# Kernel tuning notes

Hardware: AMD Instinct MI355X
Metric: run time of the kernel (lower is better)

## Reference

```python
import jax, jax.numpy as jnp
import numpy as np

N = 50000          # nodes
E = 800000         # edges (before self loops)
F_IN = 16
HID = 64
HEADS = 4
C = 64             # per-head out channels (concat=False)
G = 64             # graphs in batch
NEG_SLOPE = 0.2


def setup_inputs() -> dict:
    key = jax.random.key(0)
    ks = jax.random.split(key, 20)
    inp = {
        "x": jax.random.normal(ks[0], (N, F_IN), jnp.float32),
        "edge_index": jax.random.randint(ks[1], (2, E), 0, N, jnp.int64),
        "batch": jnp.sort(jax.random.randint(ks[2], (N,), 0, G, jnp.int64)),
        "W_in": jax.random.normal(ks[3], (HID, F_IN), jnp.float32) * 0.1,
        "b_in": jnp.zeros((HID,), jnp.float32),
        "W_out": jax.random.normal(ks[4], (1, HID), jnp.float32) * 0.1,
        "b_out": jnp.zeros((1,), jnp.float32),
    }
    for l in range(3):
        inp[f"W{l}"] = jax.random.normal(ks[5 + 4 * l], (HEADS * C, HID), jnp.float32) * 0.1
        inp[f"asrc{l}"] = jax.random.normal(ks[6 + 4 * l], (HEADS, C), jnp.float32) * 0.1
        inp[f"adst{l}"] = jax.random.normal(ks[7 + 4 * l], (HEADS, C), jnp.float32) * 0.1
        inp[f"bg{l}"] = jnp.zeros((HID,), jnp.float32)
    return inp


def _gat_layer(x, W, a_src, a_dst, bias, src, dst, n):
    # x: [N, HID] -> h: [N, HEADS, C]
    h = (x @ W.T).reshape(n, HEADS, C)
    alpha_s = jnp.einsum("nhc,hc->nh", h, a_src)   # [N, H]
    alpha_d = jnp.einsum("nhc,hc->nh", h, a_dst)
    e = jax.nn.leaky_relu(alpha_s[src] + alpha_d[dst], NEG_SLOPE)  # [E', H]
    # segment softmax over incoming edges of each dst node
    m = jax.ops.segment_max(e, dst, num_segments=n)
    e = jnp.exp(e - m[dst])
    s = jax.ops.segment_sum(e, dst, num_segments=n)
    alpha = e / (s[dst] + 1e-16)                                   # [E', H]
    msg = alpha[:, :, None] * h[src]                               # [E', H, C]
    out = jax.ops.segment_sum(msg, dst, num_segments=n)            # [N, H, C]
    return out.mean(axis=1) + bias                                 # concat=False: head mean


def reference(x, W_in, b_in, W0, asrc0, adst0, bg0, W1, asrc1, adst1, bg1,
              W2, asrc2, adst2, bg2, W_out, b_out, edge_index, batch):
    n = x.shape[0]
    # add self loops (PyG GATConv default)
    loops = jnp.arange(n, dtype=edge_index.dtype)
    src = jnp.concatenate([edge_index[0], loops])
    dst = jnp.concatenate([edge_index[1], loops])

    h = x @ W_in.T + b_in
    for W, a_s, a_d, bg in ((W0, asrc0, adst0, bg0),
                            (W1, asrc1, adst1, bg1),
                            (W2, asrc2, adst2, bg2)):
        h = jax.nn.relu(_gat_layer(h, W, a_s, a_d, bg, src, dst, n))
        # dropout p=0.2 is inactive in eval mode

    # global mean pool over graphs
    sums = jax.ops.segment_sum(h, batch, num_segments=G)
    cnt = jax.ops.segment_sum(jnp.ones((n,), h.dtype), batch, num_segments=G)
    graph_emb = sums / jnp.maximum(cnt, 1.0)[:, None]              # [G, HID]

    return jax.nn.sigmoid(graph_emb @ W_out.T + b_out)             # [G, 1]
```

## Files before the change

### kernel.cpp

```cpp
#include <hip/hip_runtime.h>
#include <hip/hip_bf16.h>
#include <hip/hip_fp16.h>

#define HID 64
#define HEADS 4
#define GCNT 64
#define F_IN 16
#define NEG 0.2f
#define NBUCK 256
#define BSLOT 6144
#define SCHUNK 2048

typedef _Float16 f16x8 __attribute__((ext_vector_type(8)));
typedef float f32x4 __attribute__((ext_vector_type(4)));

__device__ __forceinline__ unsigned pack_h2(float a, float b) {
  __half2 h = __floats2half2_rn(a, b);
  union { __half2 h; unsigned u; } c;
  c.h = h;
  return c.u;
}
__device__ __forceinline__ __half2 uas_h2(unsigned u) {
  union { unsigned u; __half2 h; } c;
  c.u = u;
  return c.h;
}
__device__ __forceinline__ unsigned h2_as_u(__half2 h) {
  union { __half2 h; unsigned u; } c;
  c.h = h;
  return c.u;
}
__device__ __forceinline__ __half2 xor16_add(__half2 v) {
  unsigned u = (unsigned)__shfl_xor((int)h2_as_u(v), 16, 64);
  return __hadd2(v, uas_h2(u));
}

__global__ __launch_bounds__(256) void k_pre(
    const float* __restrict__ W0, const float* __restrict__ asrc,
    const float* __restrict__ adst, const float* __restrict__ Win,
    const float* __restrict__ bin, int* __restrict__ bcur,
    float* __restrict__ vb, float* __restrict__ c8) {
  int t = threadIdx.x;
  if (blockIdx.x == 0) {
    bcur[t] = 0;
    return;
  }
  __shared__ float vaL[512];
#pragma unroll
  for (int it = 0; it < 2; ++it) {
    int idx = t + it * 256;
    int q = idx >> 6, j = idx & 63;
    const float* a = (q < 4) ? asrc : adst;
    int h = q & 3;
    float s = 0.f;
    for (int c = 0; c < 64; ++c) s += a[h * 64 + c] * W0[(h * 64 + c) * 64 + j];
    vaL[idx] = s;
  }
  __syncthreads();
  if (t < 128) {
    int q = t >> 4, k = t & 15;
    float s = 0.f;
    for (int j = 0; j < 64; ++j) s += vaL[q * 64 + j] * Win[j * F_IN + k];
    vb[t] = s;
  } else if (t < 136) {
    int q = t - 128;
    float s = 0.f;
    for (int j = 0; j < 64; ++j) s += vaL[q * 64 + j] * bin[j];
    c8[q] = s;
  }
}

__global__ __launch_bounds__(256) void k_bucket(
    const int* __restrict__ ei, int* __restrict__ bcur,
    unsigned* __restrict__ tmp, int E, int N) {
  __shared__ int hist[NBUCK];
  __shared__ int base[NBUCK];
  int t = threadIdx.x;
  int start = blockIdx.x * SCHUNK;
  int end = min(start + SCHUNK, E + N);
  hist[t] = 0;
  __syncthreads();
  unsigned val[8];
  int rank[8];
  bool ok[8];
#pragma unroll
  for (int k = 0; k < 8; ++k) {
    int i = start + t + k * 256;
    ok[k] = i < end;
    if (ok[k]) {
      int s, d;
      if (i < E) {
        s = ei[i];
        d = ei[E + i];
      } else {
        s = d = i - E;
      }
      val[k] = ((unsigned)d << 16) | (unsigned)s;
      rank[k] = atomicAdd(&hist[d >> 8], 1);
    }
  }
  __syncthreads();
  int h = hist[t];
  base[t] = h ? atomicAdd(&bcur[t], h) : 0;
  __syncthreads();
#pragma unroll
  for (int k = 0; k < 8; ++k) {
    if (ok[k]) {
      int bk = (int)(val[k] >> 24);
      int idx = base[bk] + rank[k];
      if (idx < BSLOT) tmp[(size_t)bk * BSLOT + idx] = val[k];
    }
  }
}

__global__ __launch_bounds__(256) void k_bsort(
    const unsigned* __restrict__ tmp, const int* __restrict__ bcur,
    int* __restrict__ rowptr, int* __restrict__ col, int N) {
  __shared__ int s[NBUCK];
  __shared__ int hist[NBUCK];
  __shared__ int pref[NBUCK];
  int b = blockIdx.x, t = threadIdx.x;
  int c = min(bcur[t], BSLOT);
  s[t] = c;
  __syncthreads();
  for (int o = 1; o < 256; o <<= 1) {
    int x = (t >= o) ? s[t - o] : 0;
    __syncthreads();
    s[t] += x;
    __syncthreads();
  }
  int base = (b == 0) ? 0 : s[b - 1];
  int total = s[255];
  int cntb = min(bcur[b], BSLOT);
  hist[t] = 0;
  __syncthreads();
  for (int j = t; j < cntb; j += 256)
    atomicAdd(&hist[(tmp[(size_t)b * BSLOT + j] >> 16) & 255], 1);
  __syncthreads();
  int v = hist[t];
  pref[t] = v;
  __syncthreads();
  for (int o = 1; o < 256; o <<= 1) {
    int x = (t >= o) ? pref[t - o] : 0;
    __syncthreads();
    pref[t] += x;
    __syncthreads();
  }
  pref[t] -= v;
  __syncthreads();
  int node = b * 256 + t;
  if (node < N) rowptr[node] = base + pref[t];
  if (b == 255 && t == 255) rowptr[N] = total;
  hist[t] = 0;
  __syncthreads();
  for (int j = t; j < cntb; j += 256) {
    unsigned e = tmp[(size_t)b * BSLOT + j];
    int d8 = (int)((e >> 16) & 255);
    int r = atomicAdd(&hist[d8], 1);
    col[base + pref[d8] + r] = (int)(e & 0xffffu);
  }
}

__global__ void k_init(const float* __restrict__ x, const float* __restrict__ Win,
                       const float* __restrict__ bin,
                       const float* __restrict__ W0, const float* __restrict__ W1,
                       const float* __restrict__ W2,
                       __half* __restrict__ Wh3, __half* __restrict__ Wcat3,
                       float* __restrict__ sums, const float* __restrict__ vb,
                       const float* __restrict__ c8,
                       float* __restrict__ as_, float* __restrict__ ad_,
                       __half* __restrict__ hh, int N) {
  int b = blockIdx.x, t = threadIdx.x;
  if (b < 384) {
    int i = b * 256 + t;
    if (i < 49152) {
      const float* W = (i < 16384) ? W0 : (i < 32768) ? W1 : W2;
      Wh3[i] = __float2half(W[i & 16383]);
    } else {
      int j = i - 49152;
      int l = j >> 14;
      int r = j & 16383;
      int c = r >> 8;
      int k256 = r & 255;
      int h = k256 & 3, kk = k256 >> 2;
      const float* W = (l == 0) ? W0 : (l == 1) ? W1 : W2;
      Wcat3[j] = __float2half(0.25f * W[(h * 64 + c) * 64 + kk]);
    }
    return;
  }
  if (b < 401) {
    int i = (b - 384) * 256 + t;
    if (i < GCNT * HID + GCNT) sums[i] = 0.f;
    return;
  }
  int i = (b - 401) * 256 + t;
  if (i >= N * HID) return;
  int n = i >> 6, j = i & 63;
  const float* xr = x + (size_t)n * F_IN;
  const float* wr = Win + j * F_IN;
  float xv[F_IN];
  float acc = bin[j];
#pragma unroll
  for (int k = 0; k < F_IN; ++k) {
    xv[k] = xr[k];
    acc = fmaf(xv[k], wr[k], acc);
  }
  hh[i] = __float2half(acc);
  if (j < 8) {
    const float* vbq = vb + j * 16;
    float s = c8[j];
#pragma unroll
    for (int k = 0; k < F_IN; ++k) s = fmaf(xv[k], vbq[k], s);
    if (j < 4) as_[(size_t)n * 4 + j] = s;
    else ad_[(size_t)n * 4 + (j - 4)] = s;
  }
}

__device__ __forceinline__ void gat_one_node(
    int node, int lane, const __half* __restrict__ h, const float* __restrict__ as_,
    const float* __restrict__ ad_, const int* __restrict__ rowptr,
    const int* __restrict__ col, __half* __restrict__ Mrow) {
  int r0 = rowptr[node];
  int deg = rowptr[node + 1] - r0;
  float4 adv = *(const float4*)(ad_ + (size_t)node * 4);

  if (deg <= 64) {
    int off = 0;
    float x0 = 0.f, x1 = 0.f, x2 = 0.f, x3 = 0.f;
    if (lane < deg) {
      int s = col[r0 + lane];
      off = s << 6;
      float4 av = *(const float4*)(as_ + (size_t)s * 4);
      float e0 = av.x + adv.x; e0 = (e0 > 0.f) ? e0 : NEG * e0;
      float e1 = av.y + adv.y; e1 = (e1 > 0.f) ? e1 : NEG * e1;
      float e2 = av.z + adv.z; e2 = (e2 > 0.f) ? e2 : NEG * e2;
      float e3 = av.w + adv.w; e3 = (e3 > 0.f) ? e3 : NEG * e3;
      x0 = __expf(fminf(e0, 60.f));
      x1 = __expf(fminf(e1, 60.f));
      x2 = __expf(fminf(e2, 60.f));
      x3 = __expf(fminf(e3, 60.f));
    }
    float s0 = x0, s1 = x1, s2 = x2, s3 = x3;
#pragma unroll
    for (int o = 32; o; o >>= 1) {
      s0 += __shfl_xor(s0, o, 64);
      s1 += __shfl_xor(s1, o, 64);
      s2 += __shfl_xor(s2, o, 64);
      s3 += __shfl_xor(s3, o, 64);
    }
    unsigned w01 = pack_h2(x0 / (s0 + 1e-16f), x1 / (s1 + 1e-16f));
    unsigned w23 = pack_h2(x2 / (s2 + 1e-16f), x3 / (s3 + 1e-16f));
    __half2 acc01 = __floats2half2_rn(0.f, 0.f);
    __half2 acc23 = acc01;
#pragma unroll 4
    for (int j = 0; j < deg; ++j) {
      int oj = __builtin_amdgcn_readlane(off, j) + lane;
      unsigned W01 = __builtin_amdgcn_readlane(w01, j);
      unsigned W23 = __builtin_amdgcn_readlane(w23, j);
      __half2 hv = __half2half2(h[oj]);
      acc01 = __hfma2(hv, uas_h2(W01), acc01);
      acc23 = __hfma2(hv, uas_h2(W23), acc23);
    }
    *(__half2*)&Mrow[lane * 4] = acc01;
    *(__half2*)&Mrow[lane * 4 + 2] = acc23;
    return;
  }
  float m0 = -1e30f, m1 = -1e30f, m2 = -1e30f, m3 = -1e30f;
  for (int j = lane; j < deg; j += 64) {
    int s = col[r0 + j];
    float4 av = *(const float4*)(as_ + (size_t)s * 4);
    float e0 = av.x + adv.x; e0 = (e0 > 0.f) ? e0 : NEG * e0; m0 = fmaxf(m0, e0);
    float e1 = av.y + adv.y; e1 = (e1 > 0.f) ? e1 : NEG * e1; m1 = fmaxf(m1, e1);
    float e2 = av.z + adv.z; e2 = (e2 > 0.f) ? e2 : NEG * e2; m2 = fmaxf(m2, e2);
    float e3 = av.w + adv.w; e3 = (e3 > 0.f) ? e3 : NEG * e3; m3 = fmaxf(m3, e3);
  }
#pragma unroll
  for (int o = 32; o; o >>= 1) {
    m0 = fmaxf(m0, __shfl_xor(m0, o, 64));
    m1 = fmaxf(m1, __shfl_xor(m1, o, 64));
    m2 = fmaxf(m2, __shfl_xor(m2, o, 64));
    m3 = fmaxf(m3, __shfl_xor(m3, o, 64));
  }
  float s0 = 0.f, s1 = 0.f, s2 = 0.f, s3 = 0.f;
  for (int j = lane; j < deg; j += 64) {
    int s = col[r0 + j];
    float4 av = *(const float4*)(as_ + (size_t)s * 4);
    float e0 = av.x + adv.x; e0 = (e0 > 0.f) ? e0 : NEG * e0; s0 += __expf(e0 - m0);
    float e1 = av.y + adv.y; e1 = (e1 > 0.f) ? e1 : NEG * e1; s1 += __expf(e1 - m1);
    float e2 = av.z + adv.z; e2 = (e2 > 0.f) ? e2 : NEG * e2; s2 += __expf(e2 - m2);
    float e3 = av.w + adv.w; e3 = (e3 > 0.f) ? e3 : NEG * e3; s3 += __expf(e3 - m3);
  }
#pragma unroll
  for (int o = 32; o; o >>= 1) {
    s0 += __shfl_xor(s0, o, 64);
    s1 += __shfl_xor(s1, o, 64);
    s2 += __shfl_xor(s2, o, 64);
    s3 += __shfl_xor(s3, o, 64);
  }
  float i0 = 1.f / (s0 + 1e-16f), i1 = 1.f / (s1 + 1e-16f);
  float i2 = 1.f / (s2 + 1e-16f), i3 = 1.f / (s3 + 1e-16f);
  float a0 = 0.f, a1 = 0.f, a2 = 0.f, a3 = 0.f;
  for (int j = 0; j < deg; ++j) {
    int s = col[r0 + j];
    float4 av = *(const float4*)(as_ + (size_t)s * 4);
    float e0 = av.x + adv.x; e0 = (e0 > 0.f) ? e0 : NEG * e0;
    float e1 = av.y + adv.y; e1 = (e1 > 0.f) ? e1 : NEG * e1;
    float e2 = av.z + adv.z; e2 = (e2 > 0.f) ? e2 : NEG * e2;
    float e3 = av.w + adv.w; e3 = (e3 > 0.f) ? e3 : NEG * e3;
    float hv = __half2float(h[(s << 6) + lane]);
    a0 = fmaf(__expf(e0 - m0) * i0, hv, a0);
    a1 = fmaf(__expf(e1 - m1) * i1, hv, a1);
    a2 = fmaf(__expf(e2 - m2) * i2, hv, a2);
    a3 = fmaf(__expf(e3 - m3) * i3, hv, a3);
  }
  *(__half2*)&Mrow[lane * 4] = __floats2half2_rn(a0, a1);
  *(__half2*)&Mrow[lane * 4 + 2] = __floats2half2_rn(a2, a3);
}

__device__ __forceinline__ void gat_pair(
    int pr, int lane, int half, int l5, int N,
    const __half* __restrict__ h, const float* __restrict__ as_,
    const float* __restrict__ ad_, const int* __restrict__ rowptr,
    const int* __restrict__ col, __half* __restrict__ Mt) {
  int n0 = pr * 2;
  int n1 = min(n0 + 1, N - 1);
  int mynode = half ? n1 : n0;
  int r0 = rowptr[mynode];
  int dg = rowptr[mynode + 1] - r0;
  int dgA = __builtin_amdgcn_readlane(dg, 0);
  int dgB = __builtin_amdgcn_readlane(dg, 32);

  if (dgA <= 32 && dgB <= 32) {
    float4 adv = *(const float4*)(ad_ + (size_t)mynode * 4);
    int off = 0;
    float x0 = 0.f, x1 = 0.f, x2 = 0.f, x3 = 0.f;
    if (l5 < dg) {
      int s = col[r0 + l5];
      off = s << 6;
      float4 av = *(const float4*)(as_ + (size_t)s * 4);
      float e0 = av.x + adv.x; e0 = (e0 > 0.f) ? e0 : NEG * e0;
      float e1 = av.y + adv.y; e1 = (e1 > 0.f) ? e1 : NEG * e1;
      float e2 = av.z + adv.z; e2 = (e2 > 0.f) ? e2 : NEG * e2;
      float e3 = av.w + adv.w; e3 = (e3 > 0.f) ? e3 : NEG * e3;
      x0 = __expf(fminf(e0, 60.f));
      x1 = __expf(fminf(e1, 60.f));
      x2 = __expf(fminf(e2, 60.f));
      x3 = __expf(fminf(e3, 60.f));
    }
    float s0 = x0, s1 = x1, s2 = x2, s3 = x3;
#pragma unroll
    for (int o = 16; o; o >>= 1) {
      s0 += __shfl_xor(s0, o, 64);
      s1 += __shfl_xor(s1, o, 64);
      s2 += __shfl_xor(s2, o, 64);
      s3 += __shfl_xor(s3, o, 64);
    }
    unsigned w01 = pack_h2(x0 / (s0 + 1e-16f), x1 / (s1 + 1e-16f));
    unsigned w23 = pack_h2(x2 / (s2 + 1e-16f), x3 / (s3 + 1e-16f));

    int g = l5 >> 4, li = l5 & 15;
    const uint2* h4p = (const uint2*)h;
    __half2 z = __floats2half2_rn(0.f, 0.f);
    __half2 a0_01 = z, a0_23 = z, a1_01 = z, a1_23 = z;
    __half2 a2_01 = z, a2_23 = z, a3_01 = z, a3_23 = z;
    int mdeg = max(dgA, dgB);
    int baddr = half << 7;
#pragma unroll 2
    for (int j = 0; j < mdeg; j += 2) {
      int addr = baddr + (j + g) * 4;
      int oj = __builtin_amdgcn_ds_bpermute(addr, off);
      unsigned W01 = (unsigned)__builtin_amdgcn_ds_bpermute(addr, (int)w01);
      unsigned W23 = (unsigned)__builtin_amdgcn_ds_bpermute(addr, (int)w23);
      uint2 hv = h4p[(oj >> 2) + li];
      __half2 ha = uas_h2(hv.x), hb = uas_h2(hv.y);
      __half2 wA = uas_h2(W01), wB = uas_h2(W23);
      __half2 c0 = __low2half2(ha), c1 = __high2half2(ha);
      __half2 c2 = __low2half2(hb), c3 = __high2half2(hb);
      a0_01 = __hfma2(c0, wA, a0_01); a0_23 = __hfma2(c0, wB, a0_23);
      a1_01 = __hfma2(c1, wA, a1_01); a1_23 = __hfma2(c1, wB, a1_23);
      a2_01 = __hfma2(c2, wA, a2_01); a2_23 = __hfma2(c2, wB, a2_23);
      a3_01 = __hfma2(c3, wA, a3_01); a3_23 = __hfma2(c3, wB, a3_23);
    }
    a0_01 = xor16_add(a0_01); a0_23 = xor16_add(a0_23);
    a1_01 = xor16_add(a1_01); a1_23 = xor16_add(a1_23);
    a2_01 = xor16_add(a2_01); a2_23 = xor16_add(a2_23);
    a3_01 = xor16_add(a3_01); a3_23 = xor16_add(a3_23);
    if (g == 0) {
      __half* row = &Mt[(mynode & 15) * 264 + li * 16];
      uint4 st1, st2;
      st1.x = h2_as_u(a0_01); st1.y = h2_as_u(a0_23);
      st1.z = h2_as_u(a1_01); st1.w = h2_as_u(a1_23);
      st2.x = h2_as_u(a2_01); st2.y = h2_as_u(a2_23);
      st2.z = h2_as_u(a3_01); st2.w = h2_as_u(a3_23);
      *(uint4*)&row[0] = st1;
      *(uint4*)&row[8] = st2;
    }
  } else {
    gat_one_node(n0, lane, h, as_, ad_, rowptr, col, &Mt[(n0 & 15) * 264]);
    if (n1 != n0) gat_one_node(n1, lane, h, as_, ad_, rowptr, col, &Mt[(n1 & 15) * 264]);
  }
}

template <bool FIN>
__global__ __launch_bounds__(256) void k_gatf(
    const __half* __restrict__ h, const float* __restrict__ as_,
    const float* __restrict__ ad_, const int* __restrict__ rowptr,
    const int* __restrict__ col, const __half* __restrict__ Wcat,
    const float* __restrict__ bg, const __half* __restrict__ Wn,
    const float* __restrict__ asrc, const float* __restrict__ adst,
    __half* __restrict__ hout, float* __restrict__ nas, float* __restrict__ nad,
    const int* __restrict__ batchv, float* __restrict__ gsums,
    int N) {
  __shared__ __half Mt[16 * 264];
  __shared__ __half O[16 * 72];
  int tid = threadIdx.x;
  int lane = tid & 63, wv = tid >> 6;
  int tile = blockIdx.x;
  int half = lane >> 5, l5 = lane & 31;
  int npairs = (N + 1) >> 1;

  int pr0 = tile * 8 + wv * 2;
  int pr1 = pr0 + 1;
  bool has0 = pr0 < npairs, has1 = pr1 < npairs;
  if (has0 && has1) {
    int my0 = min(pr0 * 2 + half, N - 1);
    int my1 = min(pr1 * 2 + half, N - 1);
    int r0a = rowptr[my0];
    int dga = rowptr[my0 + 1] - r0a;
    int r0b = rowptr[my1];
    int dgb = rowptr[my1 + 1] - r0b;
    int dA0 = __builtin_amdgcn_readlane(dga, 0);
    int dB0 = __builtin_amdgcn_readlane(dga, 32);
    int dA1 = __builtin_amdgcn_readlane(dgb, 0);
    int dB1 = __builtin_amdgcn_readlane(dgb, 32);

    if (dA0 <= 32 && dB0 <= 32 && dA1 <= 32 && dB1 <= 32) {
      float4 adva = *(const float4*)(ad_ + (size_t)my0 * 4);
      float4 advb = *(const float4*)(ad_ + (size_t)my1 * 4);
      int offa = 0, offb = 0;
      float xa0 = 0.f, xa1 = 0.f, xa2 = 0.f, xa3 = 0.f;
      float xb0 = 0.f, xb1 = 0.f, xb2 = 0.f, xb3 = 0.f;
      if (l5 < dga) {
        int s = col[r0a + l5];
        offa = s << 6;
        float4 av = *(const float4*)(as_ + (size_t)s * 4);
        float e0 = av.x + adva.x; e0 = (e0 > 0.f) ? e0 : NEG * e0;
        float e1 = av.y + adva.y; e1 = (e1 > 0.f) ? e1 : NEG * e1;
        float e2 = av.z + adva.z; e2 = (e2 > 0.f) ? e2 : NEG * e2;
        float e3 = av.w + adva.w; e3 = (e3 > 0.f) ? e3 : NEG * e3;
        xa0 = __expf(fminf(e0, 60.f));
        xa1 = __expf(fminf(e1, 60.f));
        xa2 = __expf(fminf(e2, 60.f));
        xa3 = __expf(fminf(e3, 60.f));
      }
      if (l5 < dgb) {
        int s = col[r0b + l5];
        offb = s << 6;
        float4 av = *(const float4*)(as_ + (size_t)s * 4);
        float e0 = av.x + advb.x; e0 = (e0 > 0.f) ? e0 : NEG * e0;
        float e1 = av.y + advb.y; e1 = (e1 > 0.f) ? e1 : NEG * e1;
        float e2 = av.z + advb.z; e2 = (e2 > 0.f) ? e2 : NEG * e2;
        float e3 = av.w + advb.w; e3 = (e3 > 0.f) ? e3 : NEG * e3;
        xb0 = __expf(fminf(e0, 60.f));
        xb1 = __expf(fminf(e1, 60.f));
        xb2 = __expf(fminf(e2, 60.f));
        xb3 = __expf(fminf(e3, 60.f));
      }
      float sa0 = xa0, sa1 = xa1, sa2 = xa2, sa3 = xa3;
      float sb0 = xb0, sb1 = xb1, sb2 = xb2, sb3 = xb3;
#pragma unroll
      for (int o = 16; o; o >>= 1) {
        sa0 += __shfl_xor(sa0, o, 64);
        sa1 += __shfl_xor(sa1, o, 64);
        sa2 += __shfl_xor(sa2, o, 64);
        sa3 += __shfl_xor(sa3, o, 64);
        sb0 += __shfl_xor(sb0, o, 64);
        sb1 += __shfl_xor(sb1, o, 64);
        sb2 += __shfl_xor(sb2, o, 64);
        sb3 += __shfl_xor(sb3, o, 64);
      }
      unsigned w01a = pack_h2(xa0 / (sa0 + 1e-16f), xa1 / (sa1 + 1e-16f));
      unsigned w23a = pack_h2(xa2 / (sa2 + 1e-16f), xa3 / (sa3 + 1e-16f));
      unsigned w01b = pack_h2(xb0 / (sb0 + 1e-16f), xb1 / (sb1 + 1e-16f));
      unsigned w23b = pack_h2(xb2 / (sb2 + 1e-16f), xb3 / (sb3 + 1e-16f));

      uint4* EB = (uint4*)&Mt[wv * 1056];
      EB[half * 32 + l5] = make_uint4((unsigned)offa, w01a, w23a, 0u);
      EB[64 + half * 32 + l5] = make_uint4((unsigned)offb, w01b, w23b, 0u);

      int g = l5 >> 4, li = l5 & 15;
      const uint2* h4p = (const uint2*)h;
      __half2 z = __floats2half2_rn(0.f, 0.f);
      __half2 pa0 = z, pa1 = z, pa2 = z, pa3 = z, pa4 = z, pa5 = z, pa6 = z, pa7 = z;
      __half2 pb0 = z, pb1 = z, pb2 = z, pb3 = z, pb4 = z, pb5 = z, pb6 = z, pb7 = z;
      int mm = max(max(dA0, dB0), max(dA1, dB1));
      int ebase = half * 32;
#pragma unroll 2
      for (int j = 0; j < mm; j += 2) {
        uint4 ra = EB[ebase + j + g];
        uint4 rb = EB[64 + ebase + j + g];
        uint2 hva = h4p[((int)ra.x >> 2) + li];
        uint2 hvb = h4p[((int)rb.x >> 2) + li];
        {
          __half2 ha = uas_h2(hva.x), hb = uas_h2(hva.y);
          __half2 wA = uas_h2(ra.y), wB = uas_h2(ra.z);
          __half2 c0 = __low2half2(ha), c1 = __high2half2(ha);
          __half2 c2 = __low2half2(hb), c3 = __high2half2(hb);
          pa0 = __hfma2(c0, wA, pa0); pa1 = __hfma2(c0, wB, pa1);
          pa2 = __hfma2(c1, wA, pa2); pa3 = __hfma2(c1, wB, pa3);
          pa4 = __hfma2(c2, wA, pa4); pa5 = __hfma2(c2, wB, pa5);
          pa6 = __hfma2(c3, wA, pa6); pa7 = __hfma2(c3, wB, pa7);
        }
        {
          __half2 ha = uas_h2(hvb.x), hb = uas_h2(hvb.y);
          __half2 wA = uas_h2(rb.y), wB = uas_h2(rb.z);
          __half2 c0 = __low2half2(ha), c1 = __high2half2(ha);
          __half2 c2 = __low2half2(hb), c3 = __high2half2(hb);
          pb0 = __hfma2(c0, wA, pb0); pb1 = __hfma2(c0, wB, pb1);
          pb2 = __hfma2(c1, wA, pb2); pb3 = __hfma2(c1, wB, pb3);
          pb4 = __hfma2(c2, wA, pb4); pb5 = __hfma2(c2, wB, pb5);
          pb6 = __hfma2(c3, wA, pb6); pb7 = __hfma2(c3, wB, pb7);
        }
      }
      pa0 = xor16_add(pa0); pa1 = xor16_add(pa1); pa2 = xor16_add(pa2); pa3 = xor16_add(pa3);
      pa4 = xor16_add(pa4); pa5 = xor16_add(pa5); pa6 = xor16_add(pa6); pa7 = xor16_add(pa7);
      pb0 = xor16_add(pb0); pb1 = xor16_add(pb1); pb2 = xor16_add(pb2); pb3 = xor16_add(pb3);
      pb4 = xor16_add(pb4); pb5 = xor16_add(pb5); pb6 = xor16_add(pb6); pb7 = xor16_add(pb7);
      if (g == 0) {
        __half* rowA = &Mt[(my0 & 15) * 264 + li * 16];
        __half* rowB = &Mt[(my1 & 15) * 264 + li * 16];
        uint4 s1, s2;
        s1.x = h2_as_u(pa0); s1.y = h2_as_u(pa1); s1.z = h2_as_u(pa2); s1.w = h2_as_u(pa3);
        s2.x = h2_as_u(pa4); s2.y = h2_as_u(pa5); s2.z = h2_as_u(pa6); s2.w = h2_as_u(pa7);
        *(uint4*)&rowA[0] = s1;
        *(uint4*)&rowA[8] = s2;
        s1.x = h2_as_u(pb0); s1.y = h2_as_u(pb1); s1.z = h2_as_u(pb2); s1.w = h2_as_u(pb3);
        s2.x = h2_as_u(pb4); s2.y = h2_as_u(pb5); s2.z = h2_as_u(pb6); s2.w = h2_as_u(pb7);
        *(uint4*)&rowB[0] = s1;
        *(uint4*)&rowB[8] = s2;
      }
    } else {
      gat_pair(pr0, lane, half, l5, N, h, as_, ad_, rowptr, col, Mt);
      gat_pair(pr1, lane, half, l5, N, h, as_, ad_, rowptr, col, Mt);
    }
  } else if (has0) {
    gat_pair(pr0, lane, half, l5, N, h, as_, ad_, rowptr, col, Mt);
  }
  __syncthreads();

  int quad = lane >> 4, n16 = lane & 15;
  const f16x8* WC = (const f16x8*)Wcat;
  int ch1 = wv * 16 + n16;
  float bias1 = bg[ch1];
  f32x4 c1 = {0.f, 0.f, 0.f, 0.f};
#pragma unroll
  for (int i = 0; i < 8; ++i) {
    f16x8 a = *(const f16x8*)&Mt[n16 * 264 + (i * 4 + quad) * 8];
    c1 = __builtin_amdgcn_mfma_f32_16x16x32_f16(a, WC[ch1 * 32 + i * 4 + quad], c1, 0, 0, 0);
  }
#pragma unroll
  for (int r = 0; r < 4; ++r) {
    float v = fmaxf(c1[r] + bias1, 0.f);
    O[(quad * 4 + r) * 72 + ch1] = __float2half(v);
  }
  __syncthreads();

  if (FIN) {
    if (tid < 64) {
      float* cnt_ = gsums + GCNT * HID;
      int c = tid;
      int nmax = min(16, N - tile * 16);
      int curg = -1;
      float acc = 0.f;
      int cacc = 0;
      for (int i = 0; i < nmax; ++i) {
        int gph = batchv[tile * 16 + i];
        float v = __half2float(O[i * 72 + c]);
        if (gph != curg) {
          if (curg >= 0) {
            atomicAdd(&gsums[curg * HID + c], acc);
            if (c == 0) atomicAdd(&cnt_[curg], (float)cacc);
          }
          curg = gph;
          acc = 0.f;
          cacc = 0;
        }
        acc += v;
        ++cacc;
      }
      if (curg >= 0) {
        atomicAdd(&gsums[curg * HID + c], acc);
        if (c == 0) atomicAdd(&cnt_[curg], (float)cacc);
      }
    }
    return;
  }

  {
    int nd = tid >> 4, c0 = (tid & 15) * 4;
    int node = tile * 16 + nd;
    if (node < N) {
      uint2 v = *(const uint2*)&O[nd * 72 + c0];
      *(uint2*)&hout[(size_t)node * 64 + c0] = v;
    }
  }
  {
    const f16x8* WN = (const f16x8*)Wn;
    f16x8 a0 = *(const f16x8*)&O[n16 * 72 + quad * 8];
    f16x8 a1 = *(const f16x8*)&O[n16 * 72 + 32 + quad * 8];
    f32x4 accs[4];
#pragma unroll
    for (int nt = 0; nt < 4; ++nt) {
      int ch = wv * 64 + nt * 16 + n16;
      f32x4 zz = {0.f, 0.f, 0.f, 0.f};
      zz = __builtin_amdgcn_mfma_f32_16x16x32_f16(a0, WN[ch * 8 + quad], zz, 0, 0, 0);
      zz = __builtin_amdgcn_mfma_f32_16x16x32_f16(a1, WN[ch * 8 + 4 + quad], zz, 0, 0, 0);
      accs[nt] = zz;
    }
#pragma unroll
    for (int r = 0; r < 4; ++r) {
      float vs = 0.f, vd = 0.f;
#pragma unroll
      for (int nt = 0; nt < 4; ++nt) {
        int ch = wv * 64 + nt * 16 + n16;
        vs = fmaf(accs[nt][r], asrc[ch], vs);
        vd = fmaf(accs[nt][r], adst[ch], vd);
      }
#pragma unroll
      for (int o = 8; o; o >>= 1) {
        vs += __shfl_xor(vs, o, 64);
        vd += __shfl_xor(vd, o, 64);
      }
      int node = tile * 16 + quad * 4 + r;
      if (n16 == 0 && node < N) {
        nas[(size_t)node * 4 + wv] = vs;
        nad[(size_t)node * 4 + wv] = vd;
      }
    }
  }
}

__global__ void k_out(const float* __restrict__ sums, const float* __restrict__ cnt,
                      const float* __restrict__ Wout, const float* __restrict__ bout,
                      float* __restrict__ out) {
  int g = blockIdx.x, lane = threadIdx.x;
  float cg = fmaxf(cnt[g], 1.f);
  float v = (sums[g * HID + lane] / cg) * Wout[lane];
#pragma unroll
  for (int o = 32; o; o >>= 1) v += __shfl_xor(v, o, 64);
  if (lane == 0) out[g] = 1.f / (1.f + __expf(-v));
}

extern "C" void kernel_launch(void* const* d_in, const int* in_sizes, int n_in,
                              void* d_out, int out_size, void* d_ws, size_t ws_size,
                              hipStream_t stream) {
  const float* x    = (const float*)d_in[0];
  const int*   ei   = (const int*)d_in[1];
  const int*   batch= (const int*)d_in[2];
  const float* Win  = (const float*)d_in[3];
  const float* bin  = (const float*)d_in[4];
  const float* Wout = (const float*)d_in[5];
  const float* bout = (const float*)d_in[6];
  const float* Wl[3]    = {(const float*)d_in[7],  (const float*)d_in[11], (const float*)d_in[15]};
  const float* asrcl[3] = {(const float*)d_in[8],  (const float*)d_in[12], (const float*)d_in[16]};
  const float* adstl[3] = {(const float*)d_in[9],  (const float*)d_in[13], (const float*)d_in[17]};
  const float* bgl[3]   = {(const float*)d_in[10], (const float*)d_in[14], (const float*)d_in[18]};

  int N = in_sizes[2];
  int E = in_sizes[1] / 2;
  int EE = E + N;

  char* p = (char*)d_ws;
  auto alloc = [&](size_t bytes) {
    char* r = p;
    p += (bytes + 255) & ~(size_t)255;
    return r;
  };
  int*      rowptr = (int*)alloc((size_t)(N + 1) * 4);
  int*      col    = (int*)alloc((size_t)EE * 4);
  unsigned* tmp    = (unsigned*)alloc((size_t)NBUCK * BSLOT * 4);
  int*      bcur   = (int*)alloc(NBUCK * 4);
  float*    vb     = (float*)alloc(128 * 4);
  float*    c8     = (float*)alloc(8 * 4);
  __half*   hhA    = (__half*)alloc((size_t)N * HID * 2);
  __half*   hhB    = (__half*)alloc((size_t)N * HID * 2);
  float*    asA    = (float*)alloc((size_t)N * HEADS * 4);
  float*    adA    = (float*)alloc((size_t)N * HEADS * 4);
  float*    asB    = (float*)alloc((size_t)N * HEADS * 4);
  float*    adB    = (float*)alloc((size_t)N * HEADS * 4);
  __half*   Wh3    = (__half*)alloc(3 * 16384 * 2);
  __half*   Wcat3  = (__half*)alloc(3 * 16384 * 2);
  float*    sums   = (float*)alloc((size_t)(GCNT * HID + GCNT) * 4);
  float*    cnt    = sums + GCNT * HID;

  int tiles = (N + 15) / 16;

  k_pre<<<2, 256, 0, stream>>>(Wl[0], asrcl[0], adstl[0], Win, bin, bcur, vb, c8);
  k_bucket<<<(EE + SCHUNK - 1) / SCHUNK, 256, 0, stream>>>(ei, bcur, tmp, E, N);
  k_bsort<<<NBUCK, 256, 0, stream>>>(tmp, bcur, rowptr, col, N);

  k_init<<<401 + (N * HID + 255) / 256, 256, 0, stream>>>(
      x, Win, bin, Wl[0], Wl[1], Wl[2], Wh3, Wcat3, sums, vb, c8, asA, adA, hhA, N);

  k_gatf<false><<<tiles, 256, 0, stream>>>(hhA, asA, adA, rowptr, col,
                                           Wcat3, bgl[0], Wh3 + 16384, asrcl[1], adstl[1],
                                           hhB, asB, adB, nullptr, nullptr, N);
  k_gatf<false><<<tiles, 256, 0, stream>>>(hhB, asB, adB, rowptr, col,
                                           Wcat3 + 16384, bgl[1], Wh3 + 32768, asrcl[2], adstl[2],
                                           hhA, asA, adA, nullptr, nullptr, N);
  k_gatf<true><<<tiles, 256, 0, stream>>>(hhA, asA, adA, rowptr, col,
                                          Wcat3 + 32768, bgl[2], nullptr, nullptr, nullptr,
                                          nullptr, nullptr, nullptr, batch, sums, N);

  k_out<<<GCNT, 64, 0, stream>>>(sums, cnt, Wout, bout, (float*)d_out);
}
```

Before: 314.6 us.

## Merge bucketing into init kernel and add 16-byte gather variant for GAT aggregation

Fuses the edge bucketing kernel with the feature/weight init kernel into one launch, using block-index ranges so the two independent jobs run concurrently and one launch disappears. Adds a templated aggregation variant where each lane gathers 16 bytes of a neighbour row (8 lanes per row, 4 edges per step), reducing with xor-8 and xor-16 shuffles. The wider variant is used for layers 0 and 2 and the old 8-byte path for layer 1. It uses more accumulator registers, which may lower occupancy, and clamps the edge index for padded slots.

```diff
diff --git a/kernel.cpp b/kernel.cpp
--- a/kernel.cpp
+++ b/kernel.cpp
@@ -34,6 +34,20 @@
   unsigned u = (unsigned)__shfl_xor((int)h2_as_u(v), 16, 64);
   return __hadd2(v, uas_h2(u));
 }
+__device__ __forceinline__ __half2 xor8_16_add(__half2 v) {
+  unsigned u = (unsigned)__shfl_xor((int)h2_as_u(v), 8, 64);
+  v = __hadd2(v, uas_h2(u));
+  u = (unsigned)__shfl_xor((int)h2_as_u(v), 16, 64);
+  return __hadd2(v, uas_h2(u));
+}
+
+#define EXP_U(U, W01, W23, A0, A1, A2, A3)                      \
+  do {                                                          \
+    __half2 _h = uas_h2(U);                                     \
+    __half2 _cl = __low2half2(_h), _ch = __high2half2(_h);      \
+    A0 = __hfma2(_cl, W01, A0); A1 = __hfma2(_cl, W23, A1);     \
+    A2 = __hfma2(_ch, W01, A2); A3 = __hfma2(_ch, W23, A3);     \
+  } while (0)
 
 __global__ __launch_bounds__(256) void k_pre(
     const float* __restrict__ W0, const float* __restrict__ asrc,
@@ -70,107 +84,60 @@
   }
 }
 
-__global__ __launch_bounds__(256) void k_bucket(
+__global__ __launch_bounds__(256) void k_binit(
     const int* __restrict__ ei, int* __restrict__ bcur,
-    unsigned* __restrict__ tmp, int E, int N) {
-  __shared__ int hist[NBUCK];
-  __shared__ int base[NBUCK];
+    unsigned* __restrict__ tmp, int E, int N,
+    const float* __restrict__ x, const float* __restrict__ Win,
+    const float* __restrict__ bin,
+    const float* __restrict__ W0, const float* __restrict__ W1,
+    const float* __restrict__ W2,
+    __half* __restrict__ Wh3, __half* __restrict__ Wcat3,
+    float* __restrict__ sums, const float* __restrict__ vb,
+    const float* __restrict__ c8,
+    float* __restrict__ as_, float* __restrict__ ad_,
+    __half* __restrict__ hh, int BUK) {
   int t = threadIdx.x;
-  int start = blockIdx.x * SCHUNK;
-  int end = min(start + SCHUNK, E + N);
-  hist[t] = 0;
-  __syncthreads();
-  unsigned val[8];
-  int rank[8];
-  bool ok[8];
-#pragma unroll
-  for (int k = 0; k < 8; ++k) {
-    int i = start + t + k * 256;
-    ok[k] = i < end;
-    if (ok[k]) {
-      int s, d;
-      if (i < E) {
-        s = ei[i];
-        d = ei[E + i];
-      } else {
-        s = d = i - E;
-      }
-      val[k] = ((unsigned)d << 16) | (unsigned)s;
-      rank[k] = atomicAdd(&hist[d >> 8], 1);
-    }
-  }
-  __syncthreads();
-  int h = hist[t];
-  base[t] = h ? atomicAdd(&bcur[t], h) : 0;
-  __syncthreads();
-#pragma unroll
-  for (int k = 0; k < 8; ++k) {
-    if (ok[k]) {
-      int bk = (int)(val[k] >> 24);
-      int idx = base[bk] + rank[k];
-      if (idx < BSLOT) tmp[(size_t)bk * BSLOT + idx] = val[k];
-    }
-  }
-}
-
-__global__ __launch_bounds__(256) void k_bsort(
-    const unsigned* __restrict__ tmp, const int* __restrict__ bcur,
-    int* __restrict__ rowptr, int* __restrict__ col, int N) {
-  __shared__ int s[NBUCK];
-  __shared__ int hist[NBUCK];
-  __shared__ int pref[NBUCK];
-  int b = blockIdx.x, t = threadIdx.x;
-  int c = min(bcur[t], BSLOT);
-  s[t] = c;
-  __syncthreads();
-  for (int o = 1; o < 256; o <<= 1) {
-    int x = (t >= o) ? s[t - o] : 0;
+  if (blockIdx.x < BUK) {
+    __shared__ int hist[NBUCK];
+    __shared__ int base[NBUCK];
+    int start = blockIdx.x * SCHUNK;
+    int end = min(start + SCHUNK, E + N);
+    hist[t] = 0;
     __syncthreads();
-    s[t] += x;
+    unsigned val[8];
+    int rank[8];
+    bool ok[8];
+#pragma unroll
+    for (int k = 0; k < 8; ++k) {
+      int i = start + t + k * 256;
+      ok[k] = i < end;
+      if (ok[k]) {
+        int s, d;
+        if (i < E) {
+          s = ei[i];
+          d = ei[E + i];
+        } else {
+          s = d = i - E;
+        }
+        val[k] = ((unsigned)d << 16) | (unsigned)s;
+        rank[k] = atomicAdd(&hist[d >> 8], 1);
+      }
+    }
     __syncthreads();
-  }
-  int base = (b == 0) ? 0 : s[b - 1];
-  int total = s[255];
-  int cntb = min(bcur[b], BSLOT);
-  hist[t] = 0;
-  __syncthreads();
-  for (int j = t; j < cntb; j += 256)
-    atomicAdd(&hist[(tmp[(size_t)b * BSLOT + j] >> 16) & 255], 1);
-  __syncthreads();
-  int v = hist[t];
-  pref[t] = v;
-  __syncthreads();
-  for (int o = 1; o < 256; o <<= 1) {
-    int x = (t >= o) ? pref[t - o] : 0;
+    int h = hist[t];
+    base[t] = h ? atomicAdd(&bcur[t], h) : 0;
     __syncthreads();
-    pref[t] += x;
-    __syncthreads();
-  }
-  pref[t] -= v;
-  __syncthreads();
-  int node = b * 256 + t;
-  if (node < N) rowptr[node] = base + pref[t];
-  if (b == 255 && t == 255) rowptr[N] = total;
-  hist[t] = 0;
-  __syncthreads();
-  for (int j = t; j < cntb; j += 256) {
-    unsigned e = tmp[(size_t)b * BSLOT + j];
-    int d8 = (int)((e >> 16) & 255);
-    int r = atomicAdd(&hist[d8], 1);
-    col[base + pref[d8] + r] = (int)(e & 0xffffu);
-  }
-}
-
-__global__ void k_init(const float* __restrict__ x, const float* __restrict__ Win,
-                       const float* __restrict__ bin,
-                       const float* __restrict__ W0, const float* __restrict__ W1,
-                       const float* __restrict__ W2,
-                       __half* __restrict__ Wh3, __half* __restrict__ Wcat3,
-                       float* __restrict__ sums, const float* __restrict__ vb,
-                       const float* __restrict__ c8,
-                       float* __restrict__ as_, float* __restrict__ ad_,
-                       __half* __restrict__ hh, int N) {
-  int b = blockIdx.x, t = threadIdx.x;
+#pragma unroll
+    for (int k = 0; k < 8; ++k) {
+      if (ok[k]) {
+        int bk = (int)(val[k] >> 24);
+        int idx = base[bk] + rank[k];
+        if (idx < BSLOT) tmp[(size_t)bk * BSLOT + idx] = val[k];
+      }
+    }
+    return;
+  }
+  int b = blockIdx.x - BUK;
   if (b < 384) {
     int i = b * 256 + t;
     if (i < 49152) {
@@ -213,6 +180,54 @@
     for (int k = 0; k < F_IN; ++k) s = fmaf(xv[k], vbq[k], s);
     if (j < 4) as_[(size_t)n * 4 + j] = s;
     else ad_[(size_t)n * 4 + (j - 4)] = s;
+  }
+}
+
+__global__ __launch_bounds__(256) void k_bsort(
+    const unsigned* __restrict__ tmp, const int* __restrict__ bcur,
+    int* __restrict__ rowptr, int* __restrict__ col, int N) {
+  __shared__ int s[NBUCK];
+  __shared__ int hist[NBUCK];
+  __shared__ int pref[NBUCK];
+  int b = blockIdx.x, t = threadIdx.x;
+  int c = min(bcur[t], BSLOT);
+  s[t] = c;
+  __syncthreads();
+  for (int o = 1; o < 256; o <<= 1) {
+    int x = (t >= o) ? s[t - o] : 0;
+    __syncthreads();
+    s[t] += x;
+    __syncthreads();
+  }
+  int base = (b == 0) ? 0 : s[b - 1];
+  int total = s[255];
+  int cntb = min(bcur[b], BSLOT);
+  hist[t] = 0;
+  __syncthreads();
+  for (int j = t; j < cntb; j += 256)
+    atomicAdd(&hist[(tmp[(size_t)b * BSLOT + j] >> 16) & 255], 1);
+  __syncthreads();
+  int v = hist[t];
+  pref[t] = v;
+  __syncthreads();
+  for (int o = 1; o < 256; o <<= 1) {
+    int x = (t >= o) ? pref[t - o] : 0;
+    __syncthreads();
+    pref[t] += x;
+    __syncthreads();
+  }
+  pref[t] -= v;
+  __syncthreads();
+  int node = b * 256 + t;
+  if (node < N) rowptr[node] = base + pref[t];
+  if (b == 255 && t == 255) rowptr[N] = total;
+  hist[t] = 0;
+  __syncthreads();
+  for (int j = t; j < cntb; j += 256) {
+    unsigned e = tmp[(size_t)b * BSLOT + j];
+    int d8 = (int)((e >> 16) & 255);
+    int r = atomicAdd(&hist[d8], 1);
+    col[base + pref[d8] + r] = (int)(e & 0xffffu);
   }
 }
 
@@ -401,7 +416,7 @@
   }
 }
 
-template <bool FIN>
+template <bool FIN, int GV>
 __global__ __launch_bounds__(256) void k_gatf(
     const __half* __restrict__ h, const float* __restrict__ as_,
     const float* __restrict__ ad_, const int* __restrict__ rowptr,
@@ -488,56 +503,104 @@
       EB[half * 32 + l5] = make_uint4((unsigned)offa, w01a, w23a, 0u);
       EB[64 + half * 32 + l5] = make_uint4((unsigned)offb, w01b, w23b, 0u);
 
-      int g = l5 >> 4, li = l5 & 15;
-      const uint2* h4p = (const uint2*)h;
-      __half2 z = __floats2half2_rn(0.f, 0.f);
-      __half2 pa0 = z, pa1 = z, pa2 = z, pa3 = z, pa4 = z, pa5 = z, pa6 = z, pa7 = z;
-      __half2 pb0 = z, pb1 = z, pb2 = z, pb3 = z, pb4 = z, pb5 = z, pb6 = z, pb7 = z;
       int mm = max(max(dA0, dB0), max(dA1, dB1));
-      int ebase = half * 32;
+      int eA = half * 32;
+      int eB = 64 + eA;
+
+      if (GV == 1) {
+        int grp = l5 >> 3, l3 = l5 & 7;
+        const uint4* h16 = (const uint4*)h;
+        __half2 z = __floats2half2_rn(0.f, 0.f);
+        __half2 qa[16], qb[16];
+#pragma unroll
+        for (int k = 0; k < 16; ++k) { qa[k] = z; qb[k] = z; }
 #pragma unroll 2
-      for (int j = 0; j < mm; j += 2) {
-        uint4 ra = EB[ebase + j + g];
-        uint4 rb = EB[64 + ebase + j + g];
-        uint2 hva = h4p[((int)ra.x >> 2) + li];
-        uint2 hvb = h4p[((int)rb.x >> 2) + li];
-        {
-          __half2 ha = uas_h2(hva.x), hb = uas_h2(hva.y);
-          __half2 wA = uas_h2(ra.y), wB = uas_h2(ra.z);
-          __half2 c0 = __low2half2(ha), c1 = __high2half2(ha);
-          __half2 c2 = __low2half2(hb), c3 = __high2half2(hb);
-          pa0 = __hfma2(c0, wA, pa0); pa1 = __hfma2(c0, wB, pa1);
-          pa2 = __hfma2(c1, wA, pa2); pa3 = __hfma2(c1, wB, pa3);
-          pa4 = __hfma2(c2, wA, pa4); pa5 = __hfma2(c2, wB, pa5);
-          pa6 = __hfma2(c3, wA, pa6); pa7 = __hfma2(c3, wB, pa7);
+        for (int j = 0; j < mm; j += 4) {
+          int ri = min(j + grp, 31);
+          uint4 ra = EB[eA + ri];
+          uint4 rb = EB[eB + ri];
+          uint4 va = h16[((int)ra.x >> 3) + l3];
+          uint4 vb = h16[((int)rb.x >> 3) + l3];
+          __half2 wa01 = uas_h2(ra.y), wa23 = uas_h2(ra.z);
+          __half2 wb01 = uas_h2(rb.y), wb23 = uas_h2(rb.z);
+          EXP_U(va.x, wa01, wa23, qa[0], qa[1], qa[2], qa[3]);
+          EXP_U(va.y, wa01, wa23, qa[4], qa[5], qa[6], qa[7]);
+          EXP_U(va.z, wa01, wa23, qa[8], qa[9], qa[10], qa[11]);
+          EXP_U(va.w, wa01, wa23, qa[12], qa[13], qa[14], qa[15]);
+          EXP_U(vb.x, wb01, wb23, qb[0], qb[1], qb[2], qb[3]);
+          EXP_U(vb.y, wb01, wb23, qb[4], qb[5], qb[6], qb[7]);
+          EXP_U(vb.z, wb01, wb23, qb[8], qb[9], qb[10], qb[11]);
+          EXP_U(vb.w, wb01, wb23, qb[12], qb[13], qb[14], qb[15]);
         }
-        {
-          __half2 ha = uas_h2(hvb.x), hb = uas_h2(hvb.y);
-          __half2 wA = uas_h2(rb.y), wB = uas_h2(rb.z);
-          __half2 c0 = __low2half2(ha), c1 = __high2half2(ha);
-          __half2 c2 = __low2half2(hb), c3 = __high2half2(hb);
-          pb0 = __hfma2(c0, wA, pb0); pb1 = __hfma2(c0, wB, pb1);
-          pb2 = __hfma2(c1, wA, pb2); pb3 = __hfma2(c1, wB, pb3);
-          pb4 = __hfma2(c2, wA, pb4); pb5 = __hfma2(c2, wB, pb5);
-          pb6 = __hfma2(c3, wA, pb6); pb7 = __hfma2(c3, wB, pb7);
+#pragma unroll
+        for (int k = 0; k < 16; ++k) {
+          qa[k] = xor8_16_add(qa[k]);
+          qb[k] = xor8_16_add(qb[k]);
         }
-      }
-      pa0 = xor16_add(pa0); pa1 = xor16_add(pa1); pa2 = xor16_add(pa2); pa3 = xor16_add(pa3);
-      pa4 = xor16_add(pa4); pa5 = xor16_add(pa5); pa6 = xor16_add(pa6); pa7 = xor16_add(pa7);
-      pb0 = xor16_add(pb0); pb1 = xor16_add(pb1); pb2 = xor16_add(pb2); pb3 = xor16_add(pb3);
-      pb4 = xor16_add(pb4); pb5 = xor16_add(pb5); pb6 = xor16_add(pb6); pb7 = xor16_add(pb7);
-      if (g == 0) {
-        __half* rowA = &Mt[(my0 & 15) * 264 + li * 16];
-        __half* rowB = &Mt[(my1 & 15) * 264 + li * 16];
-        uint4 s1, s2;
-        s1.x = h2_as_u(pa0); s1.y = h2_as_u(pa1); s1.z = h2_as_u(pa2); s1.w = h2_as_u(pa3);
-        s2.x = h2_as_u(pa4); s2.y = h2_as_u(pa5); s2.z = h2_as_u(pa6); s2.w = h2_as_u(pa7);
-        *(uint4*)&rowA[0] = s1;
-        *(uint4*)&rowA[8] = s2;
-        s1.x = h2_as_u(pb0); s1.y = h2_as_u(pb1); s1.z = h2_as_u(pb2); s1.w = h2_as_u(pb3);
-        s2.x = h2_as_u(pb4); s2.y = h2_as_u(pb5); s2.z = h2_as_u(pb6); s2.w = h2_as_u(pb7);
-        *(uint4*)&rowB[0] = s1;
-        *(uint4*)&rowB[8] = s2;
+        if (grp == 0) {
+          __half* rowA = &Mt[(my0 & 15) * 264 + l3 * 32];
+          __half* rowB = &Mt[(my1 & 15) * 264 + l3 * 32];
+#pragma unroll
+          for (int m = 0; m < 4; ++m) {
+            uint4 st;
+            st.x = h2_as_u(qa[m * 4 + 0]); st.y = h2_as_u(qa[m * 4 + 1]);
+            st.z = h2_as_u(qa[m * 4 + 2]); st.w = h2_as_u(qa[m * 4 + 3]);
+            *(uint4*)&rowA[m * 8] = st;
+            st.x = h2_as_u(qb[m * 4 + 0]); st.y = h2_as_u(qb[m * 4 + 1]);
+            st.z = h2_as_u(qb[m * 4 + 2]); st.w = h2_as_u(qb[m * 4 + 3]);
+            *(uint4*)&rowB[m * 8] = st;
+          }
+        }
+      } else {
+        int g = l5 >> 4, li = l5 & 15;
+        const uint2* h4p = (const uint2*)h;
+        __half2 z = __floats2half2_rn(0.f, 0.f);
+        __half2 pa0 = z, pa1 = z, pa2 = z, pa3 = z, pa4 = z, pa5 = z, pa6 = z, pa7 = z;
+        __half2 pb0 = z, pb1 = z, pb2 = z, pb3 = z, pb4 = z, pb5 = z, pb6 = z, pb7 = z;
+#pragma unroll 2
+        for (int j = 0; j < mm; j += 2) {
+          uint4 ra = EB[eA + j + g];
+          uint4 rb = EB[eB + j + g];
+          uint2 hva = h4p[((int)ra.x >> 2) + li];
+          uint2 hvb = h4p[((int)rb.x >> 2) + li];
+          {
+            __half2 ha = uas_h2(hva.x), hb = uas_h2(hva.y);
+            __half2 wA = uas_h2(ra.y), wB = uas_h2(ra.z);
+            __half2 c0 = __low2half2(ha), c1 = __high2half2(ha);
+            __half2 c2 = __low2half2(hb), c3 = __high2half2(hb);
+            pa0 = __hfma2(c0, wA, pa0); pa1 = __hfma2(c0, wB, pa1);
+            pa2 = __hfma2(c1, wA, pa2); pa3 = __hfma2(c1, wB, pa3);
+            pa4 = __hfma2(c2, wA, pa4); pa5 = __hfma2(c2, wB, pa5);
+            pa6 = __hfma2(c3, wA, pa6); pa7 = __hfma2(c3, wB, pa7);
+          }
+          {
+            __half2 ha = uas_h2(hvb.x), hb = uas_h2(hvb.y);
+            __half2 wA = uas_h2(rb.y), wB = uas_h2(rb.z);
+            __half2 c0 = __low2half2(ha), c1 = __high2half2(ha);
+            __half2 c2 = __low2half2(hb), c3 = __high2half2(hb);
+            pb0 = __hfma2(c0, wA, pb0); pb1 = __hfma2(c0, wB, pb1);
+            pb2 = __hfma2(c1, wA, pb2); pb3 = __hfma2(c1, wB, pb3);
+            pb4 = __hfma2(c2, wA, pb4); pb5 = __hfma2(c2, wB, pb5);
+            pb6 = __hfma2(c3, wA, pb6); pb7 = __hfma2(c3, wB, pb7);
+          }
+        }
+        pa0 = xor16_add(pa0); pa1 = xor16_add(pa1); pa2 = xor16_add(pa2); pa3 = xor16_add(pa3);
+        pa4 = xor16_add(pa4); pa5 = xor16_add(pa5); pa6 = xor16_add(pa6); pa7 = xor16_add(pa7);
+        pb0 = xor16_add(pb0); pb1 = xor16_add(pb1); pb2 = xor16_add(pb2); pb3 = xor16_add(pb3);
+        pb4 = xor16_add(pb4); pb5 = xor16_add(pb5); pb6 = xor16_add(pb6); pb7 = xor16_add(pb7);
+        if (g == 0) {
+          __half* rowA = &Mt[(my0 & 15) * 264 + li * 16];
+          __half* rowB = &Mt[(my1 & 15) * 264 + li * 16];
+          uint4 s1, s2;
+          s1.x = h2_as_u(pa0); s1.y = h2_as_u(pa1); s1.z = h2_as_u(pa2); s1.w = h2_as_u(pa3);
+          s2.x = h2_as_u(pa4); s2.y = h2_as_u(pa5); s2.z = h2_as_u(pa6); s2.w = h2_as_u(pa7);
+          *(uint4*)&rowA[0] = s1;
+          *(uint4*)&rowA[8] = s2;
+          s1.x = h2_as_u(pb0); s1.y = h2_as_u(pb1); s1.z = h2_as_u(pb2); s1.w = h2_as_u(pb3);
+          s2.x = h2_as_u(pb4); s2.y = h2_as_u(pb5); s2.z = h2_as_u(pb6); s2.w = h2_as_u(pb7);
+          *(uint4*)&rowB[0] = s1;
+          *(uint4*)&rowB[8] = s2;
+        }
       }
     } else {
       gat_pair(pr0, lane, half, l5, N, h, as_, ad_, rowptr, col, Mt);
@@ -694,23 +757,26 @@
   float*    cnt    = sums + GCNT * HID;
 
   int tiles = (N + 15) / 16;
+  int BUK = (EE + SCHUNK - 1) / SCHUNK;
+  int initB = 401 + (N * HID + 255) / 256;
 
   k_pre<<<2, 256, 0, stream>>>(Wl[0], asrcl[0], adstl[0], Win, bin, bcur, vb, c8);
-  k_bucket<<<(EE + SCHUNK - 1) / SCHUNK, 256, 0, stream>>>(ei, bcur, tmp, E, N);
+
+  k_binit<<<BUK + initB, 256, 0, stream>>>(ei, bcur, tmp, E, N,
+                                           x, Win, bin, Wl[0], Wl[1], Wl[2],
+                                           Wh3, Wcat3, sums, vb, c8, asA, adA, hhA, BUK);
+
   k_bsort<<<NBUCK, 256, 0, stream>>>(tmp, bcur, rowptr, col, N);
 
-  k_init<<<401 + (N * HID + 255) / 256, 256, 0, stream>>>(
-      x, Win, bin, Wl[0], Wl[1], Wl[2], Wh3, Wcat3, sums, vb, c8, asA, adA, hhA, N);
-
-  k_gatf<false><<<tiles, 256, 0, stream>>>(hhA, asA, adA, rowptr, col,
-                                           Wcat3, bgl[0], Wh3 + 16384, asrcl[1], adstl[1],
-                                           hhB, asB, adB, nullptr, nullptr, N);
-  k_gatf<false><<<tiles, 256, 0, stream>>>(hhB, asB, adB, rowptr, col,
-                                           Wcat3 + 16384, bgl[1], Wh3 + 32768, asrcl[2], adstl[2],
-                                           hhA, asA, adA, nullptr, nullptr, N);
-  k_gatf<true><<<tiles, 256, 0, stream>>>(hhA, asA, adA, rowptr, col,
-                                          Wcat3 + 32768, bgl[2], nullptr, nullptr, nullptr,
-                                          nullptr, nullptr, nullptr, batch, sums, N);
+  k_gatf<false, 1><<<tiles, 256, 0, stream>>>(hhA, asA, adA, rowptr, col,
+                                              Wcat3, bgl[0], Wh3 + 16384, asrcl[1], adstl[1],
+                                              hhB, asB, adB, nullptr, nullptr, N);
+  k_gatf<false, 0><<<tiles, 256, 0, stream>>>(hhB, asB, adB, rowptr, col,
+                                              Wcat3 + 16384, bgl[1], Wh3 + 32768, asrcl[2], adstl[2],
+                                              hhA, asA, adA, nullptr, nullptr, N);
+  k_gatf<true, 1><<<tiles, 256, 0, stream>>>(hhA, asA, adA, rowptr, col,
+                                             Wcat3 + 32768, bgl[2], nullptr, nullptr, nullptr,
+                                             nullptr, nullptr, nullptr, batch, sums, N);
 
   k_out<<<GCNT, 64, 0, stream>>>(sums, cnt, Wout, bout, (float*)d_out);
 }
```

Result: no change. 313.7 us (-0.3%).
